# Optimization experiments

Hardware: AMD Instinct MI355X
Metric: run time of the kernel (lower is better)

## Reference

```python
import jax, jax.numpy as jnp
import numpy as np


def setup_inputs() -> dict:
    key = jax.random.key(0)
    ks = jax.random.split(key, 6)
    B, N, D, E = 16, 64, 256, 256
    nodes = jax.random.normal(ks[0], (B * N, D), jnp.float32)
    edges = jax.random.normal(ks[1], (B * N * N, E), jnp.float32)
    W_in = jax.random.normal(ks[2], (2 * D + E, D), jnp.float32) / np.float32(np.sqrt(2 * D + E))
    b_in = jnp.zeros((D,), jnp.float32)
    W_coef = jax.random.normal(ks[3], (D, 1), jnp.float32) / np.float32(np.sqrt(D))
    b_coef = jnp.zeros((1,), jnp.float32)
    W_out = jax.random.normal(ks[4], (D, D), jnp.float32) / np.float32(np.sqrt(D))
    b_out = jnp.zeros((D,), jnp.float32)
    return {"nodes": nodes, "edges": edges, "W_in": W_in, "b_in": b_in,
            "W_coef": W_coef, "b_coef": b_coef, "W_out": W_out, "b_out": b_out,
            "B": B, "N": N}


def reference(nodes, edges, W_in, b_in, W_coef, b_coef, W_out, b_out, B, N):
    # Uniform nums = [N]*B special case of the ragged torch loop.
    D = nodes.shape[-1]
    n3 = nodes.reshape(B, N, D)
    # pair[b,i,j] = [node_i, node_j, edge_ij]  -> [B,N,N,2D+E]
    pair = jnp.concatenate([
        jnp.broadcast_to(n3[:, :, None, :], (B, N, N, D)),
        jnp.broadcast_to(n3[:, None, :, :], (B, N, N, D)),
        edges.reshape(B, N, N, -1),
    ], axis=-1)
    h = jax.nn.relu(pair @ W_in + b_in)            # [B,N,N,D]
    coefs = h @ W_coef + b_coef                    # [B,N,N,1]
    diag = jnp.eye(N, dtype=coefs.dtype)[None, :, :, None] * jnp.float32(1e9)
    attn = jax.nn.softmax(coefs - diag, axis=2)    # softmax over j, diag masked
    residual = jnp.sum(attn * h, axis=2)           # [B,N,D]
    new_nodes = nodes + jax.nn.relu(residual.reshape(B * N, D) @ W_out + b_out)
    return new_nodes, h.reshape(B * N * N, D)
```

## Files before the change

### kernel.cpp

```cpp
#include <hip/hip_runtime.h>
#include <hip/hip_bf16.h>

typedef unsigned int u32;
typedef unsigned short u16;
typedef __attribute__((ext_vector_type(8))) short bf16x8;
typedef __attribute__((ext_vector_type(4))) float f32x4;
typedef __attribute__((ext_vector_type(4))) float f4;

#define DI __device__ __forceinline__

DI u16 f2bfu(float f){
  union{float f; u32 i;} u; u.f = f;
  u32 lsb = (u.i >> 16) & 1u;
  u.i += 0x7fffu + lsb;
  return (u16)(u.i >> 16);
}

union BU { uint4 v; bf16x8 s; };

__global__ __launch_bounds__(256) void k_pack(const float* __restrict__ W_in,
                                              u16* __restrict__ Wp3,
                                              u16* __restrict__ Wp12)
{
  int idx = blockIdx.x * 256 + threadIdx.x;
  int l = idx & 63;
  int g = idx >> 6;
  int lq = l >> 4, lr = l & 15;
  u16 o[8];
  if (g < 128){
    int kk = g >> 4, nt = g & 15;
    int n  = nt * 16 + lr;
    int k0 = 512 + kk * 32 + lq * 8;
#pragma unroll
    for (int tt = 0; tt < 8; tt++) o[tt] = f2bfu(W_in[(size_t)(k0 + tt) * 256 + n]);
    *(uint4*)(Wp3 + (size_t)idx * 8) = *(uint4*)o;
  } else {
    int g2 = g - 128;
    int half = g2 >> 7, rem = g2 & 127;
    int nt = rem >> 3, kk = rem & 7;
    int n  = nt * 16 + lr;
    int k0 = half * 256 + kk * 32 + lq * 8;
#pragma unroll
    for (int tt = 0; tt < 8; tt++) o[tt] = f2bfu(W_in[(size_t)(k0 + tt) * 256 + n]);
    *(uint4*)(Wp12 + (size_t)g2 * 512 + (size_t)l * 8) = *(uint4*)o;
  }
}

__global__ __launch_bounds__(256) void k_pre(
    const float* __restrict__ nodes, const float* __restrict__ b_in,
    const u16* __restrict__ Wp12, float* __restrict__ P1, float* __restrict__ P2)
{
  const int t = threadIdx.x;
  const int w = t >> 6, l = t & 63, lq = l >> 4, lr = l & 15;
  const int bid = blockIdx.x;
  const int rt = bid >> 3, half = (bid >> 2) & 1, cg = bid & 3;

  bf16x8 af[8];
  {
    const float* ap = nodes + (size_t)(rt * 64 + 16 * w + lr) * 256 + lq * 8;
#pragma unroll
    for (int kk = 0; kk < 8; kk++){
      float4 x = *(const float4*)(ap + kk * 32);
      float4 y = *(const float4*)(ap + kk * 32 + 4);
      bf16x8 a;
      a[0]=(short)f2bfu(x.x); a[1]=(short)f2bfu(x.y); a[2]=(short)f2bfu(x.z); a[3]=(short)f2bfu(x.w);
      a[4]=(short)f2bfu(y.x); a[5]=(short)f2bfu(y.y); a[6]=(short)f2bfu(y.z); a[7]=(short)f2bfu(y.w);
      af[kk] = a;
    }
  }
  const uint4* wp = (const uint4*)(Wp12 + (size_t)half * 128 * 512);
  float* P = half ? P2 : P1;
#pragma unroll
  for (int ntl = 0; ntl < 4; ntl++){
    const int nt = cg * 4 + ntl;
    f32x4 acc = {0.f, 0.f, 0.f, 0.f};
#pragma unroll
    for (int kk = 0; kk < 8; kk++){
      BU bu; bu.v = wp[(nt * 8 + kk) * 64 + l];
      acc = __builtin_amdgcn_mfma_f32_16x16x32_bf16(af[kk], bu.s, acc, 0, 0, 0);
    }
    const int col = nt * 16 + lr;
    const float bv = half ? 0.f : b_in[col];
#pragma unroll
    for (int r = 0; r < 4; r++){
      const int row = rt * 64 + 16 * w + 4 * lq + r;
      P[(size_t)row * 256 + col] = acc[r] + bv;
    }
  }
}

__global__ __launch_bounds__(256, 4) void k_main(
    const float* __restrict__ nodes, const float* __restrict__ edges,
    const u16* __restrict__ Wp3, const float* __restrict__ W_coef,
    const float* __restrict__ b_coef, const float* __restrict__ W_out,
    const float* __restrict__ b_out, const float* __restrict__ P1,
    const float* __restrict__ P2, float* __restrict__ out_nodes,
    float* __restrict__ out_h)
{
  __shared__ float coefS[64];
  __shared__ float attnS[64];
  __shared__ float resS[256];

  const int t = threadIdx.x;
  const int w = t >> 6, l = t & 63, lq = l >> 4, lr = l & 15;
  const int bid = blockIdx.x;
  const int bi = ((bid & 7) << 7) | (bid >> 3);
  const int b = bi >> 6, i = bi & 63;
  const int j = 16 * w + lr;

  bf16x8 af[8];
  {
    const float* ap = edges + (size_t)bi * 16384 + (size_t)j * 256 + lq * 8;
    float4 x[8], y[8];
#pragma unroll
    for (int kk = 0; kk < 8; kk++){
      x[kk] = *(const float4*)(ap + kk * 32);
      y[kk] = *(const float4*)(ap + kk * 32 + 4);
    }
#pragma unroll
    for (int kk = 0; kk < 8; kk++){
      bf16x8 a;
      a[0]=(short)f2bfu(x[kk].x); a[1]=(short)f2bfu(x[kk].y); a[2]=(short)f2bfu(x[kk].z); a[3]=(short)f2bfu(x[kk].w);
      a[4]=(short)f2bfu(y[kk].x); a[5]=(short)f2bfu(y[kk].y); a[6]=(short)f2bfu(y[kk].z); a[7]=(short)f2bfu(y[kk].w);
      af[kk] = a;
    }
  }

  const uint4* wp = (const uint4*)Wp3;
  const float* p1p = P1 + (size_t)bi * 256;
  const float* p2p = P2 + ((size_t)b * 64 + j) * 256;
  float* hop = out_h + ((size_t)bi * 64 + j) * 256;
  float cpart = 0.f;

  for (int half = 0; half < 2; ++half){
    f32x4 acc[8];
#pragma unroll
    for (int n8 = 0; n8 < 8; n8++) acc[n8] = (f32x4){0.f, 0.f, 0.f, 0.f};
    const uint4* wph = wp + (size_t)half * 8 * 64;
#pragma unroll
    for (int n8 = 0; n8 < 8; n8++){
#pragma unroll
      for (int kk = 0; kk < 8; kk++){
        BU bu; bu.v = wph[(size_t)(kk * 16 + n8) * 64 + l];
        acc[n8] = __builtin_amdgcn_mfma_f32_16x16x32_bf16(bu.s, af[kk], acc[n8], 0, 0, 0);
      }
    }
    const int dbase = half * 128;
#pragma unroll
    for (int n8 = 0; n8 < 8; n8++){
      const int d0 = dbase + n8 * 16 + 4 * lq;
      f4 p1v = *(const f4*)(p1p + d0);
      f4 p2v = *(const f4*)(p2p + d0);
      f4 wcv = *(const f4*)(W_coef + d0);
      f4 h;
#pragma unroll
      for (int r = 0; r < 4; r++){
        float xx = acc[n8][r] + p1v[r] + p2v[r];
        h[r] = xx > 0.f ? xx : 0.f;
      }
      *(f4*)(hop + d0) = h;
      cpart += h[0]*wcv[0] + h[1]*wcv[1] + h[2]*wcv[2] + h[3]*wcv[3];
    }
  }

  cpart += __shfl_xor(cpart, 16, 64);
  cpart += __shfl_xor(cpart, 32, 64);
  if (lq == 0) coefS[j] = cpart;
  __syncthreads();

  if (t < 64){
    int jj = t;
    float val = coefS[jj] + b_coef[0] - (jj == i ? 1e9f : 0.f);
    float m = val;
#pragma unroll
    for (int off = 32; off >= 1; off >>= 1){ float o = __shfl_xor(m, off, 64); m = m > o ? m : o; }
    float e = __expf(val - m);
    float s = e;
#pragma unroll
    for (int off = 32; off >= 1; off >>= 1) s += __shfl_xor(s, off, 64);
    attnS[jj] = e / s;
  }
  __syncthreads();

  {
    const float* hb = out_h + (size_t)bi * 16384;
    float res = 0.f;
#pragma unroll 8
    for (int jj = 0; jj < 64; jj++) res += attnS[jj] * hb[(size_t)jj * 256 + t];
    resS[t] = res;
  }
  __syncthreads();

  {
    const int d = t;
    float acco = b_out[d];
#pragma unroll 8
    for (int k4 = 0; k4 < 64; k4++){
      float4 r4 = *(const float4*)&resS[k4 * 4];
      acco += r4.x * W_out[(size_t)(k4 * 4 + 0) * 256 + d];
      acco += r4.y * W_out[(size_t)(k4 * 4 + 1) * 256 + d];
      acco += r4.z * W_out[(size_t)(k4 * 4 + 2) * 256 + d];
      acco += r4.w * W_out[(size_t)(k4 * 4 + 3) * 256 + d];
    }
    float nv = nodes[(size_t)bi * 256 + d];
    out_nodes[(size_t)bi * 256 + d] = nv + (acco > 0.f ? acco : 0.f);
  }
}

extern "C" void kernel_launch(void* const* d_in, const int* in_sizes, int n_in,
                              void* d_out, int out_size, void* d_ws, size_t ws_size,
                              hipStream_t stream)
{
  const float* nodes  = (const float*)d_in[0];
  const float* edges  = (const float*)d_in[1];
  const float* W_in   = (const float*)d_in[2];
  const float* b_in   = (const float*)d_in[3];
  const float* W_coef = (const float*)d_in[4];
  const float* b_coef = (const float*)d_in[5];
  const float* W_out  = (const float*)d_in[6];
  const float* b_out  = (const float*)d_in[7];
  (void)in_sizes; (void)n_in; (void)out_size; (void)ws_size;

  float* P1  = (float*)d_ws;
  float* P2  = P1 + 262144;
  u16*  Wp3  = (u16*)(P2 + 262144);
  u16*  Wp12 = Wp3 + 65536;

  float* out_nodes = (float*)d_out;
  float* out_h = out_nodes + 262144;

  hipLaunchKernelGGL(k_pack, dim3(96),   dim3(256), 0, stream, W_in, Wp3, Wp12);
  hipLaunchKernelGGL(k_pre,  dim3(128),  dim3(256), 0, stream, nodes, b_in, Wp12, P1, P2);
  hipLaunchKernelGGL(k_main, dim3(1024), dim3(256), 0, stream,
                     nodes, edges, Wp3, W_coef, b_coef, W_out, b_out,
                     P1, P2, out_nodes, out_h);
}
```

Baseline: 190.4 us.

## Split main kernel and stage packed weights into LDS with double-buffered async loads

The fused main kernel is split into k_h, which computes h and per-edge coefficients, and k_attn, which does the softmax, attention sum and output projection, with coefficients passed through a workspace buffer. k_h repacks Wp3 in n-tile-major order and streams it into LDS chunk by chunk using global_load_lds double buffering, processing one 16-column n-tile at a time with fewer live accumulators. This aims to cut redundant per-wave global weight loads and register pressure so occupancy rises. In exchange it adds a kernel launch, a per-chunk barrier, and a re-read of h from global memory in a separate pass.

```diff
diff --git a/kernel.cpp b/kernel.cpp
--- a/kernel.cpp
+++ b/kernel.cpp
@@ -17,6 +17,12 @@
 }
 
 union BU { uint4 v; bf16x8 s; };
+
+DI void gld16(const void* g, void* l){
+  __builtin_amdgcn_global_load_lds(
+      (const __attribute__((address_space(1))) void*)g,
+      (__attribute__((address_space(3))) void*)l, 16, 0, 0);
+}
 
 __global__ __launch_bounds__(256) void k_pack(const float* __restrict__ W_in,
                                               u16* __restrict__ Wp3,
@@ -28,7 +34,7 @@
   int lq = l >> 4, lr = l & 15;
   u16 o[8];
   if (g < 128){
-    int kk = g >> 4, nt = g & 15;
+    int nt = g >> 3, kk = g & 7;
     int n  = nt * 16 + lr;
     int k0 = 512 + kk * 32 + lq * 8;
 #pragma unroll
@@ -89,88 +95,119 @@
   }
 }
 
-__global__ __launch_bounds__(256, 4) void k_main(
-    const float* __restrict__ nodes, const float* __restrict__ edges,
-    const u16* __restrict__ Wp3, const float* __restrict__ W_coef,
-    const float* __restrict__ b_coef, const float* __restrict__ W_out,
-    const float* __restrict__ b_out, const float* __restrict__ P1,
-    const float* __restrict__ P2, float* __restrict__ out_nodes,
-    float* __restrict__ out_h)
-{
-  __shared__ float coefS[64];
-  __shared__ float attnS[64];
-  __shared__ float resS[256];
+__global__ __launch_bounds__(256, 3) void k_h(
+    const float* __restrict__ edges, const u16* __restrict__ Wp3,
+    const float* __restrict__ W_coef, const float* __restrict__ P1,
+    const float* __restrict__ P2, float* __restrict__ out_h,
+    float* __restrict__ coefW)
+{
+  __shared__ uint4 wS[2][1024];
 
   const int t = threadIdx.x;
   const int w = t >> 6, l = t & 63, lq = l >> 4, lr = l & 15;
   const int bid = blockIdx.x;
   const int bi = ((bid & 7) << 7) | (bid >> 3);
-  const int b = bi >> 6, i = bi & 63;
+  const int b = bi >> 6;
   const int j = 16 * w + lr;
 
+  const char* wp3b = (const char*)Wp3;
+  auto stage = [&](int bufi, int ntc){
+    const char* src = wp3b + (size_t)ntc * 16384;
+    char* dst = (char*)&wS[bufi][0];
+#pragma unroll
+    for (int c = 0; c < 4; ++c)
+      gld16(src + (w * 4 + c) * 1024 + l * 16, dst + (w * 4 + c) * 1024);
+  };
+
+  stage(0, 0);
+
   bf16x8 af[8];
   {
     const float* ap = edges + (size_t)bi * 16384 + (size_t)j * 256 + lq * 8;
-    float4 x[8], y[8];
-#pragma unroll
-    for (int kk = 0; kk < 8; kk++){
+    float4 x[4], y[4];
+#pragma unroll
+    for (int kk = 0; kk < 4; kk++){
       x[kk] = *(const float4*)(ap + kk * 32);
       y[kk] = *(const float4*)(ap + kk * 32 + 4);
     }
 #pragma unroll
-    for (int kk = 0; kk < 8; kk++){
+    for (int kk = 0; kk < 4; kk++){
       bf16x8 a;
       a[0]=(short)f2bfu(x[kk].x); a[1]=(short)f2bfu(x[kk].y); a[2]=(short)f2bfu(x[kk].z); a[3]=(short)f2bfu(x[kk].w);
       a[4]=(short)f2bfu(y[kk].x); a[5]=(short)f2bfu(y[kk].y); a[6]=(short)f2bfu(y[kk].z); a[7]=(short)f2bfu(y[kk].w);
       af[kk] = a;
     }
-  }
-
-  const uint4* wp = (const uint4*)Wp3;
+#pragma unroll
+    for (int kk = 0; kk < 4; kk++){
+      x[kk] = *(const float4*)(ap + (kk + 4) * 32);
+      y[kk] = *(const float4*)(ap + (kk + 4) * 32 + 4);
+    }
+#pragma unroll
+    for (int kk = 0; kk < 4; kk++){
+      bf16x8 a;
+      a[0]=(short)f2bfu(x[kk].x); a[1]=(short)f2bfu(x[kk].y); a[2]=(short)f2bfu(x[kk].z); a[3]=(short)f2bfu(x[kk].w);
+      a[4]=(short)f2bfu(y[kk].x); a[5]=(short)f2bfu(y[kk].y); a[6]=(short)f2bfu(y[kk].z); a[7]=(short)f2bfu(y[kk].w);
+      af[kk + 4] = a;
+    }
+  }
+
   const float* p1p = P1 + (size_t)bi * 256;
   const float* p2p = P2 + ((size_t)b * 64 + j) * 256;
   float* hop = out_h + ((size_t)bi * 64 + j) * 256;
   float cpart = 0.f;
 
-  for (int half = 0; half < 2; ++half){
-    f32x4 acc[8];
-#pragma unroll
-    for (int n8 = 0; n8 < 8; n8++) acc[n8] = (f32x4){0.f, 0.f, 0.f, 0.f};
-    const uint4* wph = wp + (size_t)half * 8 * 64;
-#pragma unroll
-    for (int n8 = 0; n8 < 8; n8++){
+  __syncthreads();
+  int buf = 0;
+#pragma unroll
+  for (int ntc = 0; ntc < 8; ntc++){
+    if (ntc < 7) stage(buf ^ 1, ntc + 1);
+#pragma unroll
+    for (int nt2 = 0; nt2 < 2; nt2++){
+      const int nt = ntc * 2 + nt2;
+      f32x4 acc = {0.f, 0.f, 0.f, 0.f};
 #pragma unroll
       for (int kk = 0; kk < 8; kk++){
-        BU bu; bu.v = wph[(size_t)(kk * 16 + n8) * 64 + l];
-        acc[n8] = __builtin_amdgcn_mfma_f32_16x16x32_bf16(bu.s, af[kk], acc[n8], 0, 0, 0);
+        BU bu; bu.v = wS[buf][(nt2 * 8 + kk) * 64 + l];
+        acc = __builtin_amdgcn_mfma_f32_16x16x32_bf16(bu.s, af[kk], acc, 0, 0, 0);
       }
-    }
-    const int dbase = half * 128;
-#pragma unroll
-    for (int n8 = 0; n8 < 8; n8++){
-      const int d0 = dbase + n8 * 16 + 4 * lq;
+      const int d0 = nt * 16 + 4 * lq;
       f4 p1v = *(const f4*)(p1p + d0);
       f4 p2v = *(const f4*)(p2p + d0);
       f4 wcv = *(const f4*)(W_coef + d0);
       f4 h;
 #pragma unroll
       for (int r = 0; r < 4; r++){
-        float xx = acc[n8][r] + p1v[r] + p2v[r];
+        float xx = acc[r] + p1v[r] + p2v[r];
         h[r] = xx > 0.f ? xx : 0.f;
       }
       *(f4*)(hop + d0) = h;
       cpart += h[0]*wcv[0] + h[1]*wcv[1] + h[2]*wcv[2] + h[3]*wcv[3];
     }
+    __syncthreads();
+    buf ^= 1;
   }
 
   cpart += __shfl_xor(cpart, 16, 64);
   cpart += __shfl_xor(cpart, 32, 64);
-  if (lq == 0) coefS[j] = cpart;
-  __syncthreads();
+  if (lq == 0) coefW[(size_t)bi * 64 + j] = cpart;
+}
+
+__global__ __launch_bounds__(256) void k_attn(
+    const float* __restrict__ nodes, const float* __restrict__ coefW,
+    const float* __restrict__ b_coef, const float* __restrict__ W_out,
+    const float* __restrict__ b_out, const float* __restrict__ h_in,
+    float* __restrict__ out_nodes)
+{
+  __shared__ float attnS[64];
+  __shared__ float resS[256];
+
+  const int t = threadIdx.x;
+  const int bid = blockIdx.x;
+  const int bi = ((bid & 7) << 7) | (127 - (bid >> 3));
+  const int i = bi & 63;
 
   if (t < 64){
-    int jj = t;
-    float val = coefS[jj] + b_coef[0] - (jj == i ? 1e9f : 0.f);
+    float val = coefW[(size_t)bi * 64 + t] + b_coef[0] - (t == i ? 1e9f : 0.f);
     float m = val;
 #pragma unroll
     for (int off = 32; off >= 1; off >>= 1){ float o = __shfl_xor(m, off, 64); m = m > o ? m : o; }
@@ -178,12 +215,12 @@
     float s = e;
 #pragma unroll
     for (int off = 32; off >= 1; off >>= 1) s += __shfl_xor(s, off, 64);
-    attnS[jj] = e / s;
+    attnS[t] = e / s;
   }
   __syncthreads();
 
   {
-    const float* hb = out_h + (size_t)bi * 16384;
+    const float* hb = h_in + (size_t)bi * 16384;
     float res = 0.f;
 #pragma unroll 8
     for (int jj = 0; jj < 64; jj++) res += attnS[jj] * hb[(size_t)jj * 256 + t];
@@ -225,13 +262,15 @@
   float* P2  = P1 + 262144;
   u16*  Wp3  = (u16*)(P2 + 262144);
   u16*  Wp12 = Wp3 + 65536;
+  float* coefW = (float*)(Wp12 + 131072);
 
   float* out_nodes = (float*)d_out;
   float* out_h = out_nodes + 262144;
 
   hipLaunchKernelGGL(k_pack, dim3(96),   dim3(256), 0, stream, W_in, Wp3, Wp12);
   hipLaunchKernelGGL(k_pre,  dim3(128),  dim3(256), 0, stream, nodes, b_in, Wp12, P1, P2);
-  hipLaunchKernelGGL(k_main, dim3(1024), dim3(256), 0, stream,
-                     nodes, edges, Wp3, W_coef, b_coef, W_out, b_out,
-                     P1, P2, out_nodes, out_h);
-}
+  hipLaunchKernelGGL(k_h,    dim3(1024), dim3(256), 0, stream,
+                     edges, Wp3, W_coef, P1, P2, out_h, coefW);
+  hipLaunchKernelGGL(k_attn, dim3(1024), dim3(256), 0, stream,
+                     nodes, coefW, b_coef, W_out, b_out, out_h, out_nodes);
+}
```

Measured after the change: 178.2 us. 1.07x faster.
